# Kernel optimization log

Hardware: AMD Instinct MI355X
Metric: run time of the kernel (lower is better)

The kernel has to match this reference:

```python
import jax, jax.numpy as jnp
import numpy as np

EPS = 1e-08

def qmul(a, b):
    # Hamilton product on trailing dim 4 (w, x, y, z)
    aw, av = a[..., :1], a[..., 1:]
    bw, bv = b[..., :1], b[..., 1:]
    w = aw * bw - jnp.sum(av * bv, axis=-1, keepdims=True)
    v = aw * bv + bw * av + jnp.cross(av, bv)
    return jnp.concatenate([w, v], axis=-1)

def qconj(q):
    return q * jnp.array([1.0, -1.0, -1.0, -1.0], dtype=q.dtype)

def qnormalize(q):
    return q / (jnp.linalg.norm(q, axis=-1, keepdims=True) + EPS)

def exp_map(v):
    # su(2) 3-vector -> unit quaternion
    theta = jnp.linalg.norm(v, axis=-1, keepdims=True) + EPS
    axis = v / theta
    return jnp.concatenate([jnp.cos(theta), axis * jnp.sin(theta)], axis=-1)

def setup_inputs() -> dict:
    key = jax.random.key(0)
    ks = jax.random.split(key, 6)
    B, D = 2048, 4096
    Q = D // 4  # 1024 quaternions
    x = jax.random.normal(ks[0], (B, D), dtype=jnp.float32)
    state = qnormalize(jax.random.normal(ks[1], (B, Q, 4), dtype=jnp.float32))
    W_phi = jax.random.normal(ks[2], (D, D), dtype=jnp.float32) / np.sqrt(D)
    b_phi = jnp.zeros((D,), dtype=jnp.float32)
    W_dde = jax.random.normal(ks[3], (Q, D), dtype=jnp.float32) / np.sqrt(D)
    b_dde = jnp.zeros((Q,), dtype=jnp.float32)
    return {"x": x, "state": state, "W_phi": W_phi, "b_phi": b_phi,
            "W_dde": W_dde, "b_dde": b_dde}

def reference(x, state, W_phi, b_phi, W_dde, b_dde):
    B = x.shape[0]
    Q = state.shape[1]
    # phi_gate: Linear(D, D), viewed as [B, Q, 4]
    v = (jnp.einsum('bd,ed->be', x, W_phi) + b_phi).reshape(B, Q, 4)
    rotation = exp_map(v[..., 1:])
    # reversible update: S_{t+1} = normalize(S_t (x) R_t)
    next_state = qnormalize(qmul(state, rotation))
    # diagnostics (no-grad in original)
    drift = jax.lax.stop_gradient(
        jnp.mean(jnp.abs(jnp.linalg.norm(next_state, axis=-1) - 1.0)))
    eta = drift  # SpectralShiftTracker eta
    # dde gate: Linear(D, Q) + sigmoid on flattened next_state
    gate = jax.nn.sigmoid(
        jnp.einsum('bd,qd->bq', next_state.reshape(B, -1), W_dde) + b_dde)
    final_state = state + gate[..., None] * (next_state - state)
    return (final_state, eta)
```

## Files before the change

### kernel.cpp

```cpp
#include <hip/hip_runtime.h>
#include <stdint.h>

#define GLOBAL_AS __attribute__((address_space(1)))
#define LDS_AS    __attribute__((address_space(3)))

typedef __attribute__((ext_vector_type(8))) short bf16x8;
typedef __attribute__((ext_vector_type(4))) float f32x4;

#define B_DIM 2048
#define D_DIM 4096
#define Q_DIM 1024
#define EPSF  1e-8f

__device__ __forceinline__ unsigned short f2bf(float f) {
  union { float f; unsigned int u; } v; v.f = f;
  unsigned int u = v.u;
  u += 0x7FFFu + ((u >> 16) & 1u);
  return (unsigned short)(u >> 16);
}

#define NX4    2097152u
#define NWPHI4 4194304u
#define NWDDE4 1048576u

__global__ __launch_bounds__(256) void k_convert(
    const float* __restrict__ x, const float* __restrict__ wphi,
    const float* __restrict__ wdde,
    unsigned short* __restrict__ xb, unsigned short* __restrict__ wphib,
    unsigned short* __restrict__ wddeb, float* __restrict__ drift) {
  unsigned int idx = blockIdx.x * 256u + threadIdx.x;
  if (idx == 0) *drift = 0.0f;
  const float4* s; ushort4* d; unsigned int local;
  if (idx < NX4)              { s = (const float4*)x;    d = (ushort4*)xb;    local = idx; }
  else if (idx < NX4 + NWPHI4){ s = (const float4*)wphi; d = (ushort4*)wphib; local = idx - NX4; }
  else                        { s = (const float4*)wdde; d = (ushort4*)wddeb; local = idx - (NX4 + NWPHI4); }
  float4 v = s[local];
  d[local] = make_ushort4(f2bf(v.x), f2bf(v.y), f2bf(v.z), f2bf(v.w));
}


__global__ __launch_bounds__(256) void k_gemm1(
    const unsigned short* __restrict__ A, const unsigned short* __restrict__ Bm,
    const float* __restrict__ bphi, const float* __restrict__ state,
    float* __restrict__ nsf ,
    unsigned short* __restrict__ nsb ,
    float* __restrict__ drift) {
  __shared__ __align__(16) unsigned short sAB[2 * 128 * 64];
  const int t = threadIdx.x;
  const int lane = t & 63;
  const int w = t >> 6;
  const int bn = blockIdx.x;
  const int bm = blockIdx.y;
  const int rowA0 = bm * 128;
  const int rowB0 = bn * 128;

  const unsigned short* gA[4]; const unsigned short* gB[4];
  unsigned short *lA[4], *lB[4];
#pragma unroll
  for (int p = 0; p < 4; ++p) {
    const int c = t + p * 256;
    const int row = c >> 3;
    const int kcg = (c & 7) ^ (row & 7);
    gA[p] = A  + (size_t)(rowA0 + row) * D_DIM + kcg * 8;
    gB[p] = Bm + (size_t)(rowB0 + row) * D_DIM + kcg * 8;
    lA[p] = &sAB[c * 8];
    lB[p] = &sAB[8192 + c * 8];
  }

  f32x4 acc[4][4] = {};
  const int lm = lane & 15;
  const int lq = lane >> 4;
  const int mbase = (w >> 1) * 64;
  const int nbase = (w & 1) * 64;
  const int rsw = lm & 7;

  for (int k0 = 0; k0 < D_DIM; k0 += 64) {
#pragma unroll
    for (int p = 0; p < 4; ++p) {
      __builtin_amdgcn_global_load_lds((const GLOBAL_AS unsigned int*)(gA[p] + k0), (LDS_AS unsigned int*)lA[p], 16, 0, 0);
      __builtin_amdgcn_global_load_lds((const GLOBAL_AS unsigned int*)(gB[p] + k0), (LDS_AS unsigned int*)lB[p], 16, 0, 0);
    }
    __syncthreads();
#pragma unroll
    for (int ks = 0; ks < 2; ++ks) {
      const int kc = ks * 4 + lq;
      const int csw = (kc ^ rsw) * 8;
      bf16x8 af[4], bfr[4];
#pragma unroll
      for (int i = 0; i < 4; ++i)
        af[i] = *(const bf16x8*)&sAB[(mbase + i * 16 + lm) * 64 + csw];
#pragma unroll
      for (int j = 0; j < 4; ++j)
        bfr[j] = *(const bf16x8*)&sAB[8192 + (nbase + j * 16 + lm) * 64 + csw];
#pragma unroll
      for (int i = 0; i < 4; ++i)
#pragma unroll
        for (int j = 0; j < 4; ++j)
          acc[i][j] = __builtin_amdgcn_mfma_f32_16x16x32_bf16(af[i], bfr[j], acc[i][j], 0, 0, 0);
    }
    __syncthreads();
  }

  float* cscr = ((float*)sAB) + w * 1024;
  float driftLocal = 0.0f;
  const int colBase = rowB0 + nbase;
  const int qBase = colBase >> 2;
#pragma unroll
  for (int i = 0; i < 4; ++i) {
    __syncthreads();
#pragma unroll
    for (int j = 0; j < 4; ++j)
#pragma unroll
      for (int r = 0; r < 4; ++r)
        cscr[(lq * 4 + r) * 64 + j * 16 + lm] = acc[i][j][r];
    __syncthreads();
#pragma unroll
    for (int s = 0; s < 4; ++s) {
      const int qlin = s * 64 + lane;
      const int lrow = qlin >> 4;
      const int qc = qlin & 15;
      float4 vq = *(const float4*)&cscr[lrow * 64 + qc * 4];
      float4 bq = ((const float4*)bphi)[qBase + qc];
      float vx = vq.y + bq.y, vy = vq.z + bq.z, vz = vq.w + bq.w;
      float th = sqrtf(vx * vx + vy * vy + vz * vz) + EPSF;
      float st = sinf(th), ct = cosf(th);
      float sc = st / th;
      float rw = ct, rx = vx * sc, ry = vy * sc, rz = vz * sc;
      const int grow = rowA0 + mbase + i * 16 + lrow;
      const size_t qgi = (size_t)grow * Q_DIM + (qBase + qc);
      float4 sq = ((const float4*)state)[qgi];
      float aw = sq.x, ax = sq.y, ay = sq.z, az = sq.w;
      float nw = aw * rw - ax * rx - ay * ry - az * rz;
      float nx = aw * rx + rw * ax + (ay * rz - az * ry);
      float ny = aw * ry + rw * ay + (az * rx - ax * rz);
      float nz = aw * rz + rw * az + (ax * ry - ay * rx);
      float nrm = sqrtf(nw * nw + nx * nx + ny * ny + nz * nz);
      float invn = 1.0f / (nrm + EPSF);
      nw *= invn; nx *= invn; ny *= invn; nz *= invn;
      float n2 = sqrtf(nw * nw + nx * nx + ny * ny + nz * nz);
      driftLocal += fabsf(n2 - 1.0f);
      float4 o; o.x = nw; o.y = nx; o.z = ny; o.w = nz;
      ((float4*)nsf)[qgi] = o;
      ((ushort4*)nsb)[qgi] = make_ushort4(f2bf(nw), f2bf(nx), f2bf(ny), f2bf(nz));
    }
  }
#pragma unroll
  for (int off = 32; off > 0; off >>= 1) driftLocal += __shfl_down(driftLocal, off);
  if (lane == 0) atomicAdd(drift, driftLocal);
}

__global__ __launch_bounds__(256) void k_gemm2(
    const unsigned short* __restrict__ A ,
    const unsigned short* __restrict__ Bm ,
    float* __restrict__ part ) {
  __shared__ __align__(16) unsigned short sAB[2 * 128 * 64];
  const int t = threadIdx.x;
  const int lane = t & 63;
  const int w = t >> 6;
  const int bn = blockIdx.x;
  const int bm = blockIdx.y;
  const int sk = blockIdx.z;
  const int rowA0 = bm * 128;
  const int rowB0 = bn * 128;
  const int kbeg = sk * 1024;

  const unsigned short* gA[4]; const unsigned short* gB[4];
  unsigned short *lA[4], *lB[4];
#pragma unroll
  for (int p = 0; p < 4; ++p) {
    const int c = t + p * 256;
    const int row = c >> 3;
    const int kcg = (c & 7) ^ (row & 7);
    gA[p] = A  + (size_t)(rowA0 + row) * D_DIM + kbeg + kcg * 8;
    gB[p] = Bm + (size_t)(rowB0 + row) * D_DIM + kbeg + kcg * 8;
    lA[p] = &sAB[c * 8];
    lB[p] = &sAB[8192 + c * 8];
  }

  f32x4 acc[4][4] = {};
  const int lm = lane & 15;
  const int lq = lane >> 4;
  const int mbase = (w >> 1) * 64;
  const int nbase = (w & 1) * 64;
  const int rsw = lm & 7;

  for (int k0 = 0; k0 < 1024; k0 += 64) {
#pragma unroll
    for (int p = 0; p < 4; ++p) {
      __builtin_amdgcn_global_load_lds((const GLOBAL_AS unsigned int*)(gA[p] + k0), (LDS_AS unsigned int*)lA[p], 16, 0, 0);
      __builtin_amdgcn_global_load_lds((const GLOBAL_AS unsigned int*)(gB[p] + k0), (LDS_AS unsigned int*)lB[p], 16, 0, 0);
    }
    __syncthreads();
#pragma unroll
    for (int ks = 0; ks < 2; ++ks) {
      const int kc = ks * 4 + lq;
      const int csw = (kc ^ rsw) * 8;
      bf16x8 af[4], bfr[4];
#pragma unroll
      for (int i = 0; i < 4; ++i)
        af[i] = *(const bf16x8*)&sAB[(mbase + i * 16 + lm) * 64 + csw];
#pragma unroll
      for (int j = 0; j < 4; ++j)
        bfr[j] = *(const bf16x8*)&sAB[8192 + (nbase + j * 16 + lm) * 64 + csw];
#pragma unroll
      for (int i = 0; i < 4; ++i)
#pragma unroll
        for (int j = 0; j < 4; ++j)
          acc[i][j] = __builtin_amdgcn_mfma_f32_16x16x32_bf16(af[i], bfr[j], acc[i][j], 0, 0, 0);
    }
    __syncthreads();
  }

  float* pS = part + (size_t)sk * (2048u * 1024u);
#pragma unroll
  for (int i = 0; i < 4; ++i) {
    const int grow0 = rowA0 + mbase + i * 16 + lq * 4;
#pragma unroll
    for (int j = 0; j < 4; ++j) {
      const int gcol = rowB0 + nbase + j * 16 + lm;
#pragma unroll
      for (int r = 0; r < 4; ++r)
        pS[(size_t)(grow0 + r) * Q_DIM + gcol] = acc[i][j][r];
    }
  }
}

__global__ __launch_bounds__(256) void k_blend(
    const float* __restrict__ part, const float* __restrict__ bdde,
    const float* __restrict__ state, float* __restrict__ out,
    const float* __restrict__ drift, int eta_idx) {
  const unsigned int idx = blockIdx.x * 256u + threadIdx.x;
  const unsigned int q = idx & 1023u;
  float z = part[idx] + part[idx + 2097152u] + part[idx + 4194304u] +
            part[idx + 6291456u] + bdde[q];
  float gate = 1.0f / (1.0f + expf(-z));
  float4 sq = ((const float4*)state)[idx];
  float4 nq = ((const float4*)out)[idx];
  float4 f;
  f.x = sq.x + gate * (nq.x - sq.x);
  f.y = sq.y + gate * (nq.y - sq.y);
  f.z = sq.z + gate * (nq.z - sq.z);
  f.w = sq.w + gate * (nq.w - sq.w);
  ((float4*)out)[idx] = f;
  if (idx == 0) out[eta_idx] = *drift * (1.0f / 2097152.0f);
}

extern "C" void kernel_launch(void* const* d_in, const int* in_sizes, int n_in,
                              void* d_out, int out_size, void* d_ws, size_t ws_size,
                              hipStream_t stream) {
  const float* x     = (const float*)d_in[0];
  const float* state = (const float*)d_in[1];
  const float* wphi  = (const float*)d_in[2];
  const float* bphi  = (const float*)d_in[3];
  const float* wdde  = (const float*)d_in[4];
  const float* bdde  = (const float*)d_in[5];
  float* out = (float*)d_out;
  char* ws = (char*)d_ws;
  unsigned short* xb    = (unsigned short*)(ws);
  unsigned short* wphib = (unsigned short*)(ws + 16777216);
  unsigned short* wddeb = (unsigned short*)(ws + 50331648);
  unsigned short* nsb   = (unsigned short*)(ws + 58720256);
  float* drift          = (float*)(ws + 75497472);
  float* part           = (float*)(ws);

  k_convert<<<28672, 256, 0, stream>>>(x, wphi, wdde, xb, wphib, wddeb, drift);
  dim3 g1(32, 16);
  k_gemm1<<<g1, 256, 0, stream>>>(xb, wphib, bphi, state, out, nsb, drift);
  dim3 g2(8, 16, 4);
  k_gemm2<<<g2, 256, 0, stream>>>(nsb, wddeb, part);
  k_blend<<<8192, 256, 0, stream>>>(part, bdde, state, out, drift, out_size - 1);
}
```

Baseline: 321.0 us.

## Split-K the first GEMM into two halves with a separate quaternion epilogue kernel

The phi GEMM now runs as a split-K over two halves of the reduction dimension. The grid grows from 512 to 1024 blocks, which fills more of the GPU's compute units. Partial sums go to the output buffer and a workspace buffer, and a new elementwise kernel adds them with the bias and then does the exp map, quaternion product, normalization and drift reduction. The cost is an extra kernel launch and the round trip of two 32 MB fp32 partial buffers through memory. The old fused path is kept as a fallback when the workspace is too small.

```diff
diff --git a/kernel.cpp b/kernel.cpp
--- a/kernel.cpp
+++ b/kernel.cpp
@@ -149,6 +149,116 @@
   if (lane == 0) atomicAdd(drift, driftLocal);
 }
 
+__global__ __launch_bounds__(256) void k_gemm1s(
+    const unsigned short* __restrict__ A, const unsigned short* __restrict__ Bm,
+    float* __restrict__ p0, float* __restrict__ p1) {
+  __shared__ __align__(16) unsigned short sAB[2 * 128 * 64];
+  const int t = threadIdx.x;
+  const int lane = t & 63;
+  const int w = t >> 6;
+  const int bn = blockIdx.x;
+  const int bm = blockIdx.y;
+  const int sk = blockIdx.z;
+  const int rowA0 = bm * 128;
+  const int rowB0 = bn * 128;
+  const int kbeg = sk * 2048;
+
+  const unsigned short* gA[4]; const unsigned short* gB[4];
+  unsigned short *lA[4], *lB[4];
+#pragma unroll
+  for (int p = 0; p < 4; ++p) {
+    const int c = t + p * 256;
+    const int row = c >> 3;
+    const int kcg = (c & 7) ^ (row & 7);
+    gA[p] = A  + (size_t)(rowA0 + row) * D_DIM + kbeg + kcg * 8;
+    gB[p] = Bm + (size_t)(rowB0 + row) * D_DIM + kbeg + kcg * 8;
+    lA[p] = &sAB[c * 8];
+    lB[p] = &sAB[8192 + c * 8];
+  }
+
+  f32x4 acc[4][4] = {};
+  const int lm = lane & 15;
+  const int lq = lane >> 4;
+  const int mbase = (w >> 1) * 64;
+  const int nbase = (w & 1) * 64;
+  const int rsw = lm & 7;
+
+  for (int k0 = 0; k0 < 2048; k0 += 64) {
+#pragma unroll
+    for (int p = 0; p < 4; ++p) {
+      __builtin_amdgcn_global_load_lds((const GLOBAL_AS unsigned int*)(gA[p] + k0), (LDS_AS unsigned int*)lA[p], 16, 0, 0);
+      __builtin_amdgcn_global_load_lds((const GLOBAL_AS unsigned int*)(gB[p] + k0), (LDS_AS unsigned int*)lB[p], 16, 0, 0);
+    }
+    __syncthreads();
+#pragma unroll
+    for (int ks = 0; ks < 2; ++ks) {
+      const int kc = ks * 4 + lq;
+      const int csw = (kc ^ rsw) * 8;
+      bf16x8 af[4], bfr[4];
+#pragma unroll
+      for (int i = 0; i < 4; ++i)
+        af[i] = *(const bf16x8*)&sAB[(mbase + i * 16 + lm) * 64 + csw];
+#pragma unroll
+      for (int j = 0; j < 4; ++j)
+        bfr[j] = *(const bf16x8*)&sAB[8192 + (nbase + j * 16 + lm) * 64 + csw];
+#pragma unroll
+      for (int i = 0; i < 4; ++i)
+#pragma unroll
+        for (int j = 0; j < 4; ++j)
+          acc[i][j] = __builtin_amdgcn_mfma_f32_16x16x32_bf16(af[i], bfr[j], acc[i][j], 0, 0, 0);
+    }
+    __syncthreads();
+  }
+
+  float* dst = sk ? p1 : p0;
+#pragma unroll
+  for (int i = 0; i < 4; ++i) {
+    const int grow0 = rowA0 + mbase + i * 16 + lq * 4;
+#pragma unroll
+    for (int j = 0; j < 4; ++j) {
+      const int gcol = rowB0 + nbase + j * 16 + lm;
+#pragma unroll
+      for (int r = 0; r < 4; ++r)
+        dst[(size_t)(grow0 + r) * D_DIM + gcol] = acc[i][j][r];
+    }
+  }
+}
+
+__global__ __launch_bounds__(256) void k_quat(
+    const float* __restrict__ p1, const float* __restrict__ bphi,
+    const float* __restrict__ state, float* __restrict__ out,
+    unsigned short* __restrict__ nsb, float* __restrict__ drift) {
+  const unsigned int idx = blockIdx.x * 256u + threadIdx.x;
+  const unsigned int qc = idx & 1023u;
+  float4 v0 = ((const float4*)out)[idx];
+  float4 v1 = ((const float4*)p1)[idx];
+  float4 bq = ((const float4*)bphi)[qc];
+  float vx = v0.y + v1.y + bq.y;
+  float vy = v0.z + v1.z + bq.z;
+  float vz = v0.w + v1.w + bq.w;
+  float th = sqrtf(vx * vx + vy * vy + vz * vz) + EPSF;
+  float st = sinf(th), ct = cosf(th);
+  float sc = st / th;
+  float rw = ct, rx = vx * sc, ry = vy * sc, rz = vz * sc;
+  float4 sq = ((const float4*)state)[idx];
+  float aw = sq.x, ax = sq.y, ay = sq.z, az = sq.w;
+  float nw = aw * rw - ax * rx - ay * ry - az * rz;
+  float nx = aw * rx + rw * ax + (ay * rz - az * ry);
+  float ny = aw * ry + rw * ay + (az * rx - ax * rz);
+  float nz = aw * rz + rw * az + (ax * ry - ay * rx);
+  float nrm = sqrtf(nw * nw + nx * nx + ny * ny + nz * nz);
+  float invn = 1.0f / (nrm + EPSF);
+  nw *= invn; nx *= invn; ny *= invn; nz *= invn;
+  float n2 = sqrtf(nw * nw + nx * nx + ny * ny + nz * nz);
+  float driftLocal = fabsf(n2 - 1.0f);
+  float4 o; o.x = nw; o.y = nx; o.z = ny; o.w = nz;
+  ((float4*)out)[idx] = o;
+  ((ushort4*)nsb)[idx] = make_ushort4(f2bf(nw), f2bf(nx), f2bf(ny), f2bf(nz));
+#pragma unroll
+  for (int off = 32; off > 0; off >>= 1) driftLocal += __shfl_down(driftLocal, off);
+  if ((threadIdx.x & 63) == 0) atomicAdd(drift, driftLocal);
+}
+
 __global__ __launch_bounds__(256) void k_gemm2(
     const unsigned short* __restrict__ A ,
     const unsigned short* __restrict__ Bm ,
@@ -256,17 +366,36 @@
   const float* bdde  = (const float*)d_in[5];
   float* out = (float*)d_out;
   char* ws = (char*)d_ws;
-  unsigned short* xb    = (unsigned short*)(ws);
-  unsigned short* wphib = (unsigned short*)(ws + 16777216);
-  unsigned short* wddeb = (unsigned short*)(ws + 50331648);
-  unsigned short* nsb   = (unsigned short*)(ws + 58720256);
-  float* drift          = (float*)(ws + 75497472);
-  float* part           = (float*)(ws);
-
-  k_convert<<<28672, 256, 0, stream>>>(x, wphi, wdde, xb, wphib, wddeb, drift);
-  dim3 g1(32, 16);
-  k_gemm1<<<g1, 256, 0, stream>>>(xb, wphib, bphi, state, out, nsb, drift);
-  dim3 g2(8, 16, 4);
-  k_gemm2<<<g2, 256, 0, stream>>>(nsb, wddeb, part);
-  k_blend<<<8192, 256, 0, stream>>>(part, bdde, state, out, drift, out_size - 1);
-}
+
+  if (ws_size >= 109051908ull) {
+    unsigned short* xb    = (unsigned short*)(ws);
+    unsigned short* wphib = (unsigned short*)(ws + 16777216);
+    float*          p1    = (float*)(ws + 50331648);
+    unsigned short* wddeb = (unsigned short*)(ws + 83886080);
+    unsigned short* nsb   = (unsigned short*)(ws + 92274688);
+    float*          drift = (float*)(ws + 109051904);
+    float*          part  = (float*)(ws);
+
+    k_convert<<<28672, 256, 0, stream>>>(x, wphi, wdde, xb, wphib, wddeb, drift);
+    dim3 g1(32, 16, 2);
+    k_gemm1s<<<g1, 256, 0, stream>>>(xb, wphib, out, p1);
+    k_quat<<<8192, 256, 0, stream>>>(p1, bphi, state, out, nsb, drift);
+    dim3 g2(8, 16, 4);
+    k_gemm2<<<g2, 256, 0, stream>>>(nsb, wddeb, part);
+    k_blend<<<8192, 256, 0, stream>>>(part, bdde, state, out, drift, out_size - 1);
+  } else {
+    unsigned short* xb    = (unsigned short*)(ws);
+    unsigned short* wphib = (unsigned short*)(ws + 16777216);
+    unsigned short* wddeb = (unsigned short*)(ws + 50331648);
+    unsigned short* nsb   = (unsigned short*)(ws + 58720256);
+    float*          drift = (float*)(ws + 75497472);
+    float*          part  = (float*)(ws);
+
+    k_convert<<<28672, 256, 0, stream>>>(x, wphi, wdde, xb, wphib, wddeb, drift);
+    dim3 g1(32, 16);
+    k_gemm1<<<g1, 256, 0, stream>>>(xb, wphib, bphi, state, out, nsb, drift);
+    dim3 g2(8, 16, 4);
+    k_gemm2<<<g2, 256, 0, stream>>>(nsb, wddeb, part);
+    k_blend<<<8192, 256, 0, stream>>>(part, bdde, state, out, drift, out_size - 1);
+  }
+}
```

After: 709.5 us. +121.0%, slower.

## Split-K phi GEMM, separate quaternion epilogue kernel, double-buffer dde GEMM

Applied to the files above, without the earlier changes.

The phi GEMM is split into two K halves so twice as many blocks run, with partial sums written to the output buffer and a workspace buffer. A new elementwise kernel then sums the partials and applies the exp-map, quaternion product, normalisation and bf16 conversion. The dde GEMM gains a two-stage LDS double buffer so global loads overlap MFMA work. The drift atomic is replaced by per-block partial sums reduced in the blend kernel. This adds extra fp32 partial traffic and a kernel launch in exchange for better CU occupancy.

```diff
diff --git a/kernel.cpp b/kernel.cpp
--- a/kernel.cpp
+++ b/kernel.cpp
@@ -27,9 +27,8 @@
     const float* __restrict__ x, const float* __restrict__ wphi,
     const float* __restrict__ wdde,
     unsigned short* __restrict__ xb, unsigned short* __restrict__ wphib,
-    unsigned short* __restrict__ wddeb, float* __restrict__ drift) {
+    unsigned short* __restrict__ wddeb) {
   unsigned int idx = blockIdx.x * 256u + threadIdx.x;
-  if (idx == 0) *drift = 0.0f;
   const float4* s; ushort4* d; unsigned int local;
   if (idx < NX4)              { s = (const float4*)x;    d = (ushort4*)xb;    local = idx; }
   else if (idx < NX4 + NWPHI4){ s = (const float4*)wphi; d = (ushort4*)wphib; local = idx - NX4; }
@@ -39,120 +38,9 @@
 }
 
 
-__global__ __launch_bounds__(256) void k_gemm1(
+__global__ __launch_bounds__(256) void k_gemm1s(
     const unsigned short* __restrict__ A, const unsigned short* __restrict__ Bm,
-    const float* __restrict__ bphi, const float* __restrict__ state,
-    float* __restrict__ nsf ,
-    unsigned short* __restrict__ nsb ,
-    float* __restrict__ drift) {
-  __shared__ __align__(16) unsigned short sAB[2 * 128 * 64];
-  const int t = threadIdx.x;
-  const int lane = t & 63;
-  const int w = t >> 6;
-  const int bn = blockIdx.x;
-  const int bm = blockIdx.y;
-  const int rowA0 = bm * 128;
-  const int rowB0 = bn * 128;
-
-  const unsigned short* gA[4]; const unsigned short* gB[4];
-  unsigned short *lA[4], *lB[4];
-#pragma unroll
-  for (int p = 0; p < 4; ++p) {
-    const int c = t + p * 256;
-    const int row = c >> 3;
-    const int kcg = (c & 7) ^ (row & 7);
-    gA[p] = A  + (size_t)(rowA0 + row) * D_DIM + kcg * 8;
-    gB[p] = Bm + (size_t)(rowB0 + row) * D_DIM + kcg * 8;
-    lA[p] = &sAB[c * 8];
-    lB[p] = &sAB[8192 + c * 8];
-  }
-
-  f32x4 acc[4][4] = {};
-  const int lm = lane & 15;
-  const int lq = lane >> 4;
-  const int mbase = (w >> 1) * 64;
-  const int nbase = (w & 1) * 64;
-  const int rsw = lm & 7;
-
-  for (int k0 = 0; k0 < D_DIM; k0 += 64) {
-#pragma unroll
-    for (int p = 0; p < 4; ++p) {
-      __builtin_amdgcn_global_load_lds((const GLOBAL_AS unsigned int*)(gA[p] + k0), (LDS_AS unsigned int*)lA[p], 16, 0, 0);
-      __builtin_amdgcn_global_load_lds((const GLOBAL_AS unsigned int*)(gB[p] + k0), (LDS_AS unsigned int*)lB[p], 16, 0, 0);
-    }
-    __syncthreads();
-#pragma unroll
-    for (int ks = 0; ks < 2; ++ks) {
-      const int kc = ks * 4 + lq;
-      const int csw = (kc ^ rsw) * 8;
-      bf16x8 af[4], bfr[4];
-#pragma unroll
-      for (int i = 0; i < 4; ++i)
-        af[i] = *(const bf16x8*)&sAB[(mbase + i * 16 + lm) * 64 + csw];
-#pragma unroll
-      for (int j = 0; j < 4; ++j)
-        bfr[j] = *(const bf16x8*)&sAB[8192 + (nbase + j * 16 + lm) * 64 + csw];
-#pragma unroll
-      for (int i = 0; i < 4; ++i)
-#pragma unroll
-        for (int j = 0; j < 4; ++j)
-          acc[i][j] = __builtin_amdgcn_mfma_f32_16x16x32_bf16(af[i], bfr[j], acc[i][j], 0, 0, 0);
-    }
-    __syncthreads();
-  }
-
-  float* cscr = ((float*)sAB) + w * 1024;
-  float driftLocal = 0.0f;
-  const int colBase = rowB0 + nbase;
-  const int qBase = colBase >> 2;
-#pragma unroll
-  for (int i = 0; i < 4; ++i) {
-    __syncthreads();
-#pragma unroll
-    for (int j = 0; j < 4; ++j)
-#pragma unroll
-      for (int r = 0; r < 4; ++r)
-        cscr[(lq * 4 + r) * 64 + j * 16 + lm] = acc[i][j][r];
-    __syncthreads();
-#pragma unroll
-    for (int s = 0; s < 4; ++s) {
-      const int qlin = s * 64 + lane;
-      const int lrow = qlin >> 4;
-      const int qc = qlin & 15;
-      float4 vq = *(const float4*)&cscr[lrow * 64 + qc * 4];
-      float4 bq = ((const float4*)bphi)[qBase + qc];
-      float vx = vq.y + bq.y, vy = vq.z + bq.z, vz = vq.w + bq.w;
-      float th = sqrtf(vx * vx + vy * vy + vz * vz) + EPSF;
-      float st = sinf(th), ct = cosf(th);
-      float sc = st / th;
-      float rw = ct, rx = vx * sc, ry = vy * sc, rz = vz * sc;
-      const int grow = rowA0 + mbase + i * 16 + lrow;
-      const size_t qgi = (size_t)grow * Q_DIM + (qBase + qc);
-      float4 sq = ((const float4*)state)[qgi];
-      float aw = sq.x, ax = sq.y, ay = sq.z, az = sq.w;
-      float nw = aw * rw - ax * rx - ay * ry - az * rz;
-      float nx = aw * rx + rw * ax + (ay * rz - az * ry);
-      float ny = aw * ry + rw * ay + (az * rx - ax * rz);
-      float nz = aw * rz + rw * az + (ax * ry - ay * rx);
-      float nrm = sqrtf(nw * nw + nx * nx + ny * ny + nz * nz);
-      float invn = 1.0f / (nrm + EPSF);
-      nw *= invn; nx *= invn; ny *= invn; nz *= invn;
-      float n2 = sqrtf(nw * nw + nx * nx + ny * ny + nz * nz);
-      driftLocal += fabsf(n2 - 1.0f);
-      float4 o; o.x = nw; o.y = nx; o.z = ny; o.w = nz;
-      ((float4*)nsf)[qgi] = o;
-      ((ushort4*)nsb)[qgi] = make_ushort4(f2bf(nw), f2bf(nx), f2bf(ny), f2bf(nz));
-    }
-  }
-#pragma unroll
-  for (int off = 32; off > 0; off >>= 1) driftLocal += __shfl_down(driftLocal, off);
-  if (lane == 0) atomicAdd(drift, driftLocal);
-}
-
-__global__ __launch_bounds__(256) void k_gemm2(
-    const unsigned short* __restrict__ A ,
-    const unsigned short* __restrict__ Bm ,
-    float* __restrict__ part ) {
+    float* __restrict__ p0, float* __restrict__ p1) {
   __shared__ __align__(16) unsigned short sAB[2 * 128 * 64];
   const int t = threadIdx.x;
   const int lane = t & 63;
@@ -162,7 +50,7 @@
   const int sk = blockIdx.z;
   const int rowA0 = bm * 128;
   const int rowB0 = bn * 128;
-  const int kbeg = sk * 1024;
+  const int kbeg = sk * 2048;
 
   const unsigned short* gA[4]; const unsigned short* gB[4];
   unsigned short *lA[4], *lB[4];
@@ -184,7 +72,7 @@
   const int nbase = (w & 1) * 64;
   const int rsw = lm & 7;
 
-  for (int k0 = 0; k0 < 1024; k0 += 64) {
+  for (int k0 = 0; k0 < 2048; k0 += 64) {
 #pragma unroll
     for (int p = 0; p < 4; ++p) {
       __builtin_amdgcn_global_load_lds((const GLOBAL_AS unsigned int*)(gA[p] + k0), (LDS_AS unsigned int*)lA[p], 16, 0, 0);
@@ -211,6 +99,133 @@
     __syncthreads();
   }
 
+  float* dst = sk ? p1 : p0;
+#pragma unroll
+  for (int i = 0; i < 4; ++i) {
+    const int grow0 = rowA0 + mbase + i * 16 + lq * 4;
+#pragma unroll
+    for (int j = 0; j < 4; ++j) {
+      const int gcol = rowB0 + nbase + j * 16 + lm;
+#pragma unroll
+      for (int r = 0; r < 4; ++r)
+        dst[(size_t)(grow0 + r) * D_DIM + gcol] = acc[i][j][r];
+    }
+  }
+}
+
+__global__ __launch_bounds__(256) void k_quat(
+    const float* __restrict__ p1, const float* __restrict__ bphi,
+    const float* __restrict__ state, float* __restrict__ out,
+    unsigned short* __restrict__ nsb, float* __restrict__ driftPart) {
+  __shared__ float sW[4];
+  const unsigned int idx = blockIdx.x * 256u + threadIdx.x;
+  const unsigned int qc = idx & 1023u;
+  float4 v0 = ((const float4*)out)[idx];
+  float4 v1 = ((const float4*)p1)[idx];
+  float4 bq = ((const float4*)bphi)[qc];
+  float vx = v0.y + v1.y + bq.y;
+  float vy = v0.z + v1.z + bq.z;
+  float vz = v0.w + v1.w + bq.w;
+  float th = sqrtf(vx * vx + vy * vy + vz * vz) + EPSF;
+  float st = sinf(th), ct = cosf(th);
+  float sc = st / th;
+  float rw = ct, rx = vx * sc, ry = vy * sc, rz = vz * sc;
+  float4 sq = ((const float4*)state)[idx];
+  float aw = sq.x, ax = sq.y, ay = sq.z, az = sq.w;
+  float nw = aw * rw - ax * rx - ay * ry - az * rz;
+  float nx = aw * rx + rw * ax + (ay * rz - az * ry);
+  float ny = aw * ry + rw * ay + (az * rx - ax * rz);
+  float nz = aw * rz + rw * az + (ax * ry - ay * rx);
+  float nrm = sqrtf(nw * nw + nx * nx + ny * ny + nz * nz);
+  float invn = 1.0f / (nrm + EPSF);
+  nw *= invn; nx *= invn; ny *= invn; nz *= invn;
+  float n2 = sqrtf(nw * nw + nx * nx + ny * ny + nz * nz);
+  float driftLocal = fabsf(n2 - 1.0f);
+  float4 o; o.x = nw; o.y = nx; o.z = ny; o.w = nz;
+  ((float4*)out)[idx] = o;
+  ((ushort4*)nsb)[idx] = make_ushort4(f2bf(nw), f2bf(nx), f2bf(ny), f2bf(nz));
+#pragma unroll
+  for (int off = 32; off > 0; off >>= 1) driftLocal += __shfl_down(driftLocal, off);
+  if ((threadIdx.x & 63) == 0) sW[threadIdx.x >> 6] = driftLocal;
+  __syncthreads();
+  if (threadIdx.x == 0)
+    driftPart[blockIdx.x] = sW[0] + sW[1] + sW[2] + sW[3];
+}
+
+__global__ __launch_bounds__(256) void k_gemm2(
+    const unsigned short* __restrict__ A ,
+    const unsigned short* __restrict__ Bm ,
+    float* __restrict__ part ) {
+  __shared__ __align__(16) unsigned short sAB[2][2 * 128 * 64];
+  const int t = threadIdx.x;
+  const int lane = t & 63;
+  const int w = t >> 6;
+  const int bn = blockIdx.x;
+  const int bm = blockIdx.y;
+  const int sk = blockIdx.z;
+  const int rowA0 = bm * 128;
+  const int rowB0 = bn * 128;
+  const int kbeg = sk * 1024;
+
+  const unsigned short* gA[4]; const unsigned short* gB[4];
+  int cOff[4];
+#pragma unroll
+  for (int p = 0; p < 4; ++p) {
+    const int c = t + p * 256;
+    const int row = c >> 3;
+    const int kcg = (c & 7) ^ (row & 7);
+    gA[p] = A  + (size_t)(rowA0 + row) * D_DIM + kbeg + kcg * 8;
+    gB[p] = Bm + (size_t)(rowB0 + row) * D_DIM + kbeg + kcg * 8;
+    cOff[p] = c * 8;
+  }
+
+  f32x4 acc[4][4] = {};
+  const int lm = lane & 15;
+  const int lq = lane >> 4;
+  const int mbase = (w >> 1) * 64;
+  const int nbase = (w & 1) * 64;
+  const int rsw = lm & 7;
+
+#pragma unroll
+  for (int p = 0; p < 4; ++p) {
+    __builtin_amdgcn_global_load_lds((const GLOBAL_AS unsigned int*)(gA[p]), (LDS_AS unsigned int*)&sAB[0][cOff[p]], 16, 0, 0);
+    __builtin_amdgcn_global_load_lds((const GLOBAL_AS unsigned int*)(gB[p]), (LDS_AS unsigned int*)&sAB[0][8192 + cOff[p]], 16, 0, 0);
+  }
+  __syncthreads();
+
+  int cur = 0;
+  for (int tstep = 0; tstep < 16; ++tstep) {
+    if (tstep < 15) {
+      const int kn = (tstep + 1) * 64;
+      const int nb = cur ^ 1;
+#pragma unroll
+      for (int p = 0; p < 4; ++p) {
+        __builtin_amdgcn_global_load_lds((const GLOBAL_AS unsigned int*)(gA[p] + kn), (LDS_AS unsigned int*)&sAB[nb][cOff[p]], 16, 0, 0);
+        __builtin_amdgcn_global_load_lds((const GLOBAL_AS unsigned int*)(gB[p] + kn), (LDS_AS unsigned int*)&sAB[nb][8192 + cOff[p]], 16, 0, 0);
+      }
+    }
+    const unsigned short* sbase = sAB[cur];
+#pragma unroll
+    for (int ks = 0; ks < 2; ++ks) {
+      const int kc = ks * 4 + lq;
+      const int csw = (kc ^ rsw) * 8;
+      bf16x8 af[4], bfr[4];
+#pragma unroll
+      for (int i = 0; i < 4; ++i)
+        af[i] = *(const bf16x8*)&sbase[(mbase + i * 16 + lm) * 64 + csw];
+#pragma unroll
+      for (int j = 0; j < 4; ++j)
+        bfr[j] = *(const bf16x8*)&sbase[8192 + (nbase + j * 16 + lm) * 64 + csw];
+#pragma unroll
+      for (int i = 0; i < 4; ++i)
+#pragma unroll
+        for (int j = 0; j < 4; ++j)
+          acc[i][j] = __builtin_amdgcn_mfma_f32_16x16x32_bf16(af[i], bfr[j], acc[i][j], 0, 0, 0);
+    }
+    __syncthreads();
+    cur ^= 1;
+  }
+
   float* pS = part + (size_t)sk * (2048u * 1024u);
 #pragma unroll
   for (int i = 0; i < 4; ++i) {
@@ -228,11 +243,13 @@
 __global__ __launch_bounds__(256) void k_blend(
     const float* __restrict__ part, const float* __restrict__ bdde,
     const float* __restrict__ state, float* __restrict__ out,
-    const float* __restrict__ drift, int eta_idx) {
+    const float* __restrict__ driftPart, int eta_idx) {
+  __shared__ float sW[4];
   const unsigned int idx = blockIdx.x * 256u + threadIdx.x;
   const unsigned int q = idx & 1023u;
-  float z = part[idx] + part[idx + 2097152u] + part[idx + 4194304u] +
-            part[idx + 6291456u] + bdde[q];
+  float z = bdde[q];
+#pragma unroll
+  for (int k = 0; k < 4; ++k) z += part[idx + k * 2097152u];
   float gate = 1.0f / (1.0f + expf(-z));
   float4 sq = ((const float4*)state)[idx];
   float4 nq = ((const float4*)out)[idx];
@@ -242,7 +259,16 @@
   f.z = sq.z + gate * (nq.z - sq.z);
   f.w = sq.w + gate * (nq.w - sq.w);
   ((float4*)out)[idx] = f;
-  if (idx == 0) out[eta_idx] = *drift * (1.0f / 2097152.0f);
+  if (blockIdx.x == 0) {
+    float s = 0.0f;
+    for (int k = threadIdx.x; k < 8192; k += 256) s += driftPart[k];
+#pragma unroll
+    for (int off = 32; off > 0; off >>= 1) s += __shfl_down(s, off);
+    if ((threadIdx.x & 63) == 0) sW[threadIdx.x >> 6] = s;
+    __syncthreads();
+    if (threadIdx.x == 0)
+      out[eta_idx] = (sW[0] + sW[1] + sW[2] + sW[3]) * (1.0f / 2097152.0f);
+  }
 }
 
 extern "C" void kernel_launch(void* const* d_in, const int* in_sizes, int n_in,
@@ -256,17 +282,20 @@
   const float* bdde  = (const float*)d_in[5];
   float* out = (float*)d_out;
   char* ws = (char*)d_ws;
+
   unsigned short* xb    = (unsigned short*)(ws);
   unsigned short* wphib = (unsigned short*)(ws + 16777216);
-  unsigned short* wddeb = (unsigned short*)(ws + 50331648);
-  unsigned short* nsb   = (unsigned short*)(ws + 58720256);
-  float* drift          = (float*)(ws + 75497472);
-  float* part           = (float*)(ws);
-
-  k_convert<<<28672, 256, 0, stream>>>(x, wphi, wdde, xb, wphib, wddeb, drift);
-  dim3 g1(32, 16);
-  k_gemm1<<<g1, 256, 0, stream>>>(xb, wphib, bphi, state, out, nsb, drift);
+  float*          p1    = (float*)(ws + 50331648);
+  unsigned short* wddeb = (unsigned short*)(ws + 83886080);
+  unsigned short* nsb   = (unsigned short*)(ws + 92274688);
+  float*          driftPart = (float*)(ws);
+  float*          part  = (float*)(ws + 32768);
+
+  k_convert<<<28672, 256, 0, stream>>>(x, wphi, wdde, xb, wphib, wddeb);
+  dim3 g1(32, 16, 2);
+  k_gemm1s<<<g1, 256, 0, stream>>>(xb, wphib, out, p1);
+  k_quat<<<8192, 256, 0, stream>>>(p1, bphi, state, out, nsb, driftPart);
   dim3 g2(8, 16, 4);
   k_gemm2<<<g2, 256, 0, stream>>>(nsb, wddeb, part);
-  k_blend<<<8192, 256, 0, stream>>>(part, bdde, state, out, drift, out_size - 1);
-}
+  k_blend<<<8192, 256, 0, stream>>>(part, bdde, state, out, driftPart, out_size - 1);
+}
```

Result: no change. 317.8 us (-1.0%).
